# Performance work log

Measured on AMD Instinct MI355X. Metric: run time of the kernel, lower is better.

## Reference

```python
import jax, jax.numpy as jnp
import numpy as np

NUM_NODES = 200000
NUM_EDGES = 200000
NUM_GRAPHS = 2048
F_IN = 128
H = 64


def setup_inputs() -> dict:
    key = jax.random.key(0)
    ks = jax.random.split(key, 16)
    x = jax.random.normal(ks[0], (NUM_NODES, F_IN), dtype=jnp.float32)
    edge_index = jax.random.randint(ks[1], (2, NUM_EDGES), 0, NUM_NODES, dtype=jnp.int64)
    batch = jnp.sort(jax.random.randint(ks[2], (NUM_NODES,), 0, NUM_GRAPHS, dtype=jnp.int64))
    s_in = 1.0 / np.sqrt(F_IN)
    s_h = 1.0 / np.sqrt(H)
    W1a = jax.random.uniform(ks[3], (F_IN, H), jnp.float32, -s_in, s_in)
    b1a = jax.random.uniform(ks[4], (H,), jnp.float32, -s_in, s_in)
    W1b = jax.random.uniform(ks[5], (H, H), jnp.float32, -s_h, s_h)
    b1b = jax.random.uniform(ks[6], (H,), jnp.float32, -s_h, s_h)
    W2a = jax.random.uniform(ks[7], (H, H), jnp.float32, -s_h, s_h)
    b2a = jax.random.uniform(ks[8], (H,), jnp.float32, -s_h, s_h)
    W2b = jax.random.uniform(ks[9], (H, H), jnp.float32, -s_h, s_h)
    b2b = jax.random.uniform(ks[10], (H,), jnp.float32, -s_h, s_h)
    fcW = jax.random.uniform(ks[11], (H, 1), jnp.float32, -s_h, s_h)
    fcb = jax.random.uniform(ks[12], (1,), jnp.float32, -s_h, s_h)
    return {"x": x, "edge_index": edge_index, "batch": batch,
            "W1a": W1a, "b1a": b1a, "W1b": W1b, "b1b": b1b,
            "W2a": W2a, "b2a": b2a, "W2b": W2b, "b2b": b2b,
            "fcW": fcW, "fcb": fcb}


def gin_conv(h, edge_index, Wa, ba, Wb, bb):
    # sum aggregation: messages from source (row 0) scattered to target (row 1)
    msgs = h[edge_index[0]]  # [E, D]
    agg = jax.ops.segment_sum(msgs, edge_index[1], num_segments=NUM_NODES)
    z = h + agg  # eps = 0 default: (1+eps)*x + sum_j x_j
    z = jnp.maximum(z @ Wa + ba, 0.0)
    return z @ Wb + bb


def reference(x, edge_index, batch, W1a, b1a, W1b, b1b, W2a, b2a, W2b, b2b, fcW, fcb):
    h = jnp.maximum(gin_conv(x, edge_index, W1a, b1a, W1b, b1b), 0.0)
    h = jnp.maximum(gin_conv(h, edge_index, W2a, b2a, W2b, b2b), 0.0)
    # global mean pool per graph
    sums = jax.ops.segment_sum(h, batch, num_segments=NUM_GRAPHS)  # [G, H]
    counts = jax.ops.segment_sum(jnp.ones((h.shape[0],), h.dtype), batch, num_segments=NUM_GRAPHS)
    pooled = sums / jnp.maximum(counts, 1.0)[:, None]
    out = pooled @ fcW + fcb  # [G, 1]
    return out.squeeze(-1)
```

## Files before the change

### kernel.cpp

```cpp
#include <hip/hip_runtime.h>
#include <hip/hip_bf16.h>


#define NODES 200000
#define NPAD  200064
#define EDGES 200000
#define GRAPHS 2048
#define NB_SCAN 782

typedef __attribute__((ext_vector_type(8))) short short8;
typedef __attribute__((ext_vector_type(4))) float f32x4;

__device__ __forceinline__ unsigned short f2bf(float f) {
    unsigned u = __builtin_bit_cast(unsigned, f);
    u = (u + 0x7fffu + ((u >> 16) & 1u)) >> 16;
    return (unsigned short)u;
}
__device__ __forceinline__ float bf2f(unsigned short h) {
    unsigned u = ((unsigned)h) << 16;
    return __builtin_bit_cast(float, u);
}

__global__ __launch_bounds__(256) void count_k(
    const int* __restrict__ ei, int* __restrict__ cnt, int E)
{
    int e = blockIdx.x * 256 + threadIdx.x;
    if (e < E) atomicAdd(&cnt[ei[E + e]], 1);
}

__global__ __launch_bounds__(256) void scan1_k(
    const int* __restrict__ cnt, int* __restrict__ excl,
    int* __restrict__ bsum, int N)
{
    __shared__ int sh[256];
    int tid = threadIdx.x;
    int i = blockIdx.x * 256 + tid;
    int v = (i < N) ? cnt[i] : 0;
    sh[tid] = v;
    __syncthreads();
    for (int off = 1; off < 256; off <<= 1) {
        int t = (tid >= off) ? sh[tid - off] : 0;
        __syncthreads();
        sh[tid] += t;
        __syncthreads();
    }
    if (i < N) excl[i] = sh[tid] - v;
    if (tid == 255) bsum[blockIdx.x] = sh[255];
}

__global__ __launch_bounds__(1024) void scan2_k(int* __restrict__ bsum, int NB)
{
    __shared__ int sh[1024];
    int tid = threadIdx.x;
    int v = (tid < NB) ? bsum[tid] : 0;
    sh[tid] = v;
    __syncthreads();
    for (int off = 1; off < 1024; off <<= 1) {
        int t = (tid >= off) ? sh[tid - off] : 0;
        __syncthreads();
        sh[tid] += t;
        __syncthreads();
    }
    if (tid < NB) bsum[tid] = sh[tid] - v;
}

__global__ __launch_bounds__(256) void scan3_k(
    int* __restrict__ rowptr, const int* __restrict__ bsum,
    int* __restrict__ cursor, int N, int E)
{
    int i = blockIdx.x * 256 + threadIdx.x;
    if (i < N) {
        int v = rowptr[i] + bsum[blockIdx.x];
        rowptr[i] = v;
        cursor[i] = v;
    }
    if (i == 0) rowptr[N] = E;
}

__global__ __launch_bounds__(256) void fill_k(
    const int* __restrict__ ei, int* __restrict__ cursor,
    int* __restrict__ srcs, int E)
{
    int e = blockIdx.x * 256 + threadIdx.x;
    if (e < E) {
        int d = ei[E + e];
        int p = atomicAdd(&cursor[d], 1);
        srcs[p] = ei[e];
    }
}

__device__ __forceinline__ void wconv(const float* __restrict__ W,
                                      short* __restrict__ F, int e, int NE)
{
    int lane = e & 63, nb = (e >> 6) & 3, kc = e >> 8;
    int col = nb * 16 + (lane & 15);
    int kb = kc * 32 + ((lane >> 4) * 8);
    short8 hi, lo;
    #pragma unroll
    for (int j = 0; j < 8; ++j) {
        float w = W[(size_t)(kb + j) * 64 + col];
        unsigned short h = f2bf(w);
        float r = w - bf2f(h);
        hi[j] = (short)h;
        lo[j] = (short)f2bf(r);
    }
    *reinterpret_cast<short8*>(F + (size_t)e * 8) = hi;
    *reinterpret_cast<short8*>(F + (size_t)NE * 8 + (size_t)e * 8) = lo;
}

__global__ __launch_bounds__(256) void wsplit_k(
    const float* __restrict__ W1a, const float* __restrict__ W1b,
    const float* __restrict__ W2a, const float* __restrict__ W2b,
    short* __restrict__ F1a, short* __restrict__ F1b,
    short* __restrict__ F2a, short* __restrict__ F2b)
{
    int t = blockIdx.x * 256 + threadIdx.x;
    if (t < 1024)      wconv(W1a, F1a, t, 1024);
    else if (t < 1536) wconv(W1b, F1b, t - 1024, 512);
    else if (t < 2048) wconv(W2a, F2a, t - 1536, 512);
    else if (t < 2560) wconv(W2b, F2b, t - 2048, 512);
}

__device__ __forceinline__ void cvt_a8(const float4& a, const float4& b,
                                       short8& hi, short8& lo)
{
    float av[8] = {a.x, a.y, a.z, a.w, b.x, b.y, b.z, b.w};
    #pragma unroll
    for (int j = 0; j < 8; ++j) {
        unsigned short h = f2bf(av[j]);
        float r = av[j] - bf2f(h);
        hi[j] = (short)h;
        lo[j] = (short)f2bf(r);
    }
}

__global__ __launch_bounds__(256) void mm1_k(
    const float* __restrict__ A, const short* __restrict__ Wf,
    float* __restrict__ out, int N)
{
    const int tid = threadIdx.x;
    const int lane = tid & 63;
    const int wv = tid >> 6;
    const int row0w = blockIdx.x * 128 + wv * 32;
    const int grp = lane >> 4, c = lane & 15;
    const int koff = grp * 8;

    const float* Ar0 = A + (size_t)min(row0w + c, N - 1) * 128;
    const float* Ar1 = A + (size_t)min(row0w + 16 + c, N - 1) * 128;

    f32x4 acc[2][4];
    #pragma unroll
    for (int rg = 0; rg < 2; ++rg)
        #pragma unroll
        for (int nb = 0; nb < 4; ++nb)
            acc[rg][nb] = (f32x4){0.f, 0.f, 0.f, 0.f};

    #pragma unroll
    for (int kc = 0; kc < 4; ++kc) {
        const int kb = kc * 32 + koff;
        float4 a00 = *reinterpret_cast<const float4*>(Ar0 + kb);
        float4 a01 = *reinterpret_cast<const float4*>(Ar0 + kb + 4);
        float4 a10 = *reinterpret_cast<const float4*>(Ar1 + kb);
        float4 a11 = *reinterpret_cast<const float4*>(Ar1 + kb + 4);
        short8 h0, l0, h1, l1;
        cvt_a8(a00, a01, h0, l0);
        cvt_a8(a10, a11, h1, l1);
        #pragma unroll
        for (int nb = 0; nb < 4; ++nb) {
            short8 whi = *reinterpret_cast<const short8*>(Wf + ((size_t)((kc * 4 + nb) * 64) + lane) * 8);
            short8 wlo = *reinterpret_cast<const short8*>(Wf + ((size_t)(1024 + (kc * 4 + nb) * 64) + lane) * 8);
            acc[0][nb] = __builtin_amdgcn_mfma_f32_16x16x32_bf16(h0, whi, acc[0][nb], 0, 0, 0);
            acc[0][nb] = __builtin_amdgcn_mfma_f32_16x16x32_bf16(l0, whi, acc[0][nb], 0, 0, 0);
            acc[0][nb] = __builtin_amdgcn_mfma_f32_16x16x32_bf16(h0, wlo, acc[0][nb], 0, 0, 0);
            acc[1][nb] = __builtin_amdgcn_mfma_f32_16x16x32_bf16(h1, whi, acc[1][nb], 0, 0, 0);
            acc[1][nb] = __builtin_amdgcn_mfma_f32_16x16x32_bf16(l1, whi, acc[1][nb], 0, 0, 0);
            acc[1][nb] = __builtin_amdgcn_mfma_f32_16x16x32_bf16(h1, wlo, acc[1][nb], 0, 0, 0);
        }
    }

    #pragma unroll
    for (int rg = 0; rg < 2; ++rg)
        #pragma unroll
        for (int nb = 0; nb < 4; ++nb)
            #pragma unroll
            for (int reg = 0; reg < 4; ++reg)
                out[(size_t)(row0w + rg * 16 + grp * 4 + reg) * 64 + nb * 16 + c] = acc[rg][nb][reg];
}

__device__ __forceinline__ void agg_frag16(
    const float* __restrict__ y, const int* __restrict__ rowptr,
    const int* __restrict__ srcs, const float* __restrict__ bias,
    int n, int koff, bool valid, short8 fh[2], short8 fl[2])
{
    if (!valid) {
        #pragma unroll
        for (int i = 0; i < 8; ++i) {
            fh[0][i] = 0; fl[0][i] = 0; fh[1][i] = 0; fl[1][i] = 0;
        }
        return;
    }
    float a[16];
    {
        const float* yr = y + (size_t)n * 64;
        float4 a0 = *reinterpret_cast<const float4*>(yr + koff);
        float4 a1 = *reinterpret_cast<const float4*>(yr + koff + 4);
        float4 a2 = *reinterpret_cast<const float4*>(yr + 32 + koff);
        float4 a3 = *reinterpret_cast<const float4*>(yr + 32 + koff + 4);
        float4 b0 = *reinterpret_cast<const float4*>(bias + koff);
        float4 b1 = *reinterpret_cast<const float4*>(bias + koff + 4);
        float4 b2 = *reinterpret_cast<const float4*>(bias + 32 + koff);
        float4 b3 = *reinterpret_cast<const float4*>(bias + 32 + koff + 4);
        a[0] = a0.x + b0.x;  a[1] = a0.y + b0.y;  a[2] = a0.z + b0.z;  a[3] = a0.w + b0.w;
        a[4] = a1.x + b1.x;  a[5] = a1.y + b1.y;  a[6] = a1.z + b1.z;  a[7] = a1.w + b1.w;
        a[8] = a2.x + b2.x;  a[9] = a2.y + b2.y;  a[10] = a2.z + b2.z; a[11] = a2.w + b2.w;
        a[12] = a3.x + b3.x; a[13] = a3.y + b3.y; a[14] = a3.z + b3.z; a[15] = a3.w + b3.w;
    }
    int s0 = rowptr[n], s1 = rowptr[n + 1];
    for (int j = s0; j < s1; ++j) {
        const float* ys = y + (size_t)srcs[j] * 64;
        float4 v0 = *reinterpret_cast<const float4*>(ys + koff);
        float4 v1 = *reinterpret_cast<const float4*>(ys + koff + 4);
        float4 v2 = *reinterpret_cast<const float4*>(ys + 32 + koff);
        float4 v3 = *reinterpret_cast<const float4*>(ys + 32 + koff + 4);
        a[0] += v0.x;  a[1] += v0.y;  a[2] += v0.z;  a[3] += v0.w;
        a[4] += v1.x;  a[5] += v1.y;  a[6] += v1.z;  a[7] += v1.w;
        a[8] += v2.x;  a[9] += v2.y;  a[10] += v2.z; a[11] += v2.w;
        a[12] += v3.x; a[13] += v3.y; a[14] += v3.z; a[15] += v3.w;
    }
    #pragma unroll
    for (int i = 0; i < 16; ++i) {
        float v = fmaxf(a[i], 0.f);
        unsigned short h = f2bf(v);
        float r = v - bf2f(h);
        fh[i >> 3][i & 7] = (short)h;
        fl[i >> 3][i & 7] = (short)f2bf(r);
    }
}

__global__ __launch_bounds__(256) void mmaggmm_k(
    const float* __restrict__ y, const int* __restrict__ rowptr,
    const int* __restrict__ srcs, const float* __restrict__ bagg,
    const short* __restrict__ Wf1, const float* __restrict__ b1,
    const short* __restrict__ Wf2, float* __restrict__ out, int N)
{
    __shared__ short hT[4][32 * 72];
    __shared__ short lT[4][32 * 72];
    const int tid = threadIdx.x;
    const int lane = tid & 63;
    const int wv = tid >> 6;
    const int row0w = blockIdx.x * 128 + wv * 32;
    const int grp = lane >> 4, c = lane & 15;
    const int koff = grp * 8;

    short8 fh0[2], fl0[2], fh1[2], fl1[2];
    {
        int n0 = row0w + c;
        int n1 = row0w + 16 + c;
        agg_frag16(y, rowptr, srcs, bagg, n0, koff, n0 < N, fh0, fl0);
        agg_frag16(y, rowptr, srcs, bagg, n1, koff, n1 < N, fh1, fl1);
    }

    f32x4 acc[2][4];
    #pragma unroll
    for (int rg = 0; rg < 2; ++rg)
        #pragma unroll
        for (int nb = 0; nb < 4; ++nb)
            acc[rg][nb] = (f32x4){0.f, 0.f, 0.f, 0.f};

    #pragma unroll
    for (int kc = 0; kc < 2; ++kc) {
        #pragma unroll
        for (int nb = 0; nb < 4; ++nb) {
            short8 whi = *reinterpret_cast<const short8*>(Wf1 + ((size_t)((kc * 4 + nb) * 64) + lane) * 8);
            short8 wlo = *reinterpret_cast<const short8*>(Wf1 + ((size_t)(512 + (kc * 4 + nb) * 64) + lane) * 8);
            acc[0][nb] = __builtin_amdgcn_mfma_f32_16x16x32_bf16(fh0[kc], whi, acc[0][nb], 0, 0, 0);
            acc[0][nb] = __builtin_amdgcn_mfma_f32_16x16x32_bf16(fl0[kc], whi, acc[0][nb], 0, 0, 0);
            acc[0][nb] = __builtin_amdgcn_mfma_f32_16x16x32_bf16(fh0[kc], wlo, acc[0][nb], 0, 0, 0);
            acc[1][nb] = __builtin_amdgcn_mfma_f32_16x16x32_bf16(fh1[kc], whi, acc[1][nb], 0, 0, 0);
            acc[1][nb] = __builtin_amdgcn_mfma_f32_16x16x32_bf16(fl1[kc], whi, acc[1][nb], 0, 0, 0);
            acc[1][nb] = __builtin_amdgcn_mfma_f32_16x16x32_bf16(fh1[kc], wlo, acc[1][nb], 0, 0, 0);
        }
    }

    #pragma unroll
    for (int rg = 0; rg < 2; ++rg)
        #pragma unroll
        for (int nb = 0; nb < 4; ++nb) {
            const int col = nb * 16 + c;
            const float bv = b1[col];
            #pragma unroll
            for (int reg = 0; reg < 4; ++reg) {
                const int lr = rg * 16 + grp * 4 + reg;
                float v = fmaxf(acc[rg][nb][reg] + bv, 0.f);
                unsigned short h = f2bf(v);
                float r = v - bf2f(h);
                hT[wv][lr * 72 + col] = (short)h;
                lT[wv][lr * 72 + col] = (short)f2bf(r);
            }
        }
    __syncthreads();

    f32x4 acc2[2][4];
    #pragma unroll
    for (int rg = 0; rg < 2; ++rg)
        #pragma unroll
        for (int nb = 0; nb < 4; ++nb)
            acc2[rg][nb] = (f32x4){0.f, 0.f, 0.f, 0.f};

    #pragma unroll
    for (int kc = 0; kc < 2; ++kc) {
        const int kb = kc * 32 + koff;
        short8 h0 = *reinterpret_cast<const short8*>(&hT[wv][(0 + c) * 72 + kb]);
        short8 l0 = *reinterpret_cast<const short8*>(&lT[wv][(0 + c) * 72 + kb]);
        short8 h1 = *reinterpret_cast<const short8*>(&hT[wv][(16 + c) * 72 + kb]);
        short8 l1 = *reinterpret_cast<const short8*>(&lT[wv][(16 + c) * 72 + kb]);
        #pragma unroll
        for (int nb = 0; nb < 4; ++nb) {
            short8 whi = *reinterpret_cast<const short8*>(Wf2 + ((size_t)((kc * 4 + nb) * 64) + lane) * 8);
            short8 wlo = *reinterpret_cast<const short8*>(Wf2 + ((size_t)(512 + (kc * 4 + nb) * 64) + lane) * 8);
            acc2[0][nb] = __builtin_amdgcn_mfma_f32_16x16x32_bf16(h0, whi, acc2[0][nb], 0, 0, 0);
            acc2[0][nb] = __builtin_amdgcn_mfma_f32_16x16x32_bf16(l0, whi, acc2[0][nb], 0, 0, 0);
            acc2[0][nb] = __builtin_amdgcn_mfma_f32_16x16x32_bf16(h0, wlo, acc2[0][nb], 0, 0, 0);
            acc2[1][nb] = __builtin_amdgcn_mfma_f32_16x16x32_bf16(h1, whi, acc2[1][nb], 0, 0, 0);
            acc2[1][nb] = __builtin_amdgcn_mfma_f32_16x16x32_bf16(l1, whi, acc2[1][nb], 0, 0, 0);
            acc2[1][nb] = __builtin_amdgcn_mfma_f32_16x16x32_bf16(h1, wlo, acc2[1][nb], 0, 0, 0);
        }
    }

    #pragma unroll
    for (int rg = 0; rg < 2; ++rg)
        #pragma unroll
        for (int nb = 0; nb < 4; ++nb)
            #pragma unroll
            for (int reg = 0; reg < 4; ++reg)
                out[(size_t)(row0w + rg * 16 + grp * 4 + reg) * 64 + nb * 16 + c] = acc2[rg][nb][reg];
}

__global__ __launch_bounds__(256) void mmaggpool_k(
    const float* __restrict__ y, const int* __restrict__ rowptr,
    const int* __restrict__ srcs, const float* __restrict__ bagg,
    const short* __restrict__ Wf, const float* __restrict__ bias,
    const float* __restrict__ fcW, const int* __restrict__ batch,
    float* __restrict__ gacc, int N)
{
    __shared__ float rd[4][32];
    __shared__ int bls[4][32];
    const int tid = threadIdx.x;
    const int lane = tid & 63;
    const int wv = tid >> 6;
    const int row0w = blockIdx.x * 128 + wv * 32;
    const int grp = lane >> 4, c = lane & 15;
    const int koff = grp * 8;

    short8 fh0[2], fl0[2], fh1[2], fl1[2];
    {
        int n0 = row0w + c;
        int n1 = row0w + 16 + c;
        agg_frag16(y, rowptr, srcs, bagg, n0, koff, n0 < N, fh0, fl0);
        agg_frag16(y, rowptr, srcs, bagg, n1, koff, n1 < N, fh1, fl1);
    }

    f32x4 acc[2][4];
    #pragma unroll
    for (int rg = 0; rg < 2; ++rg)
        #pragma unroll
        for (int nb = 0; nb < 4; ++nb)
            acc[rg][nb] = (f32x4){0.f, 0.f, 0.f, 0.f};

    #pragma unroll
    for (int kc = 0; kc < 2; ++kc) {
        #pragma unroll
        for (int nb = 0; nb < 4; ++nb) {
            short8 whi = *reinterpret_cast<const short8*>(Wf + ((size_t)((kc * 4 + nb) * 64) + lane) * 8);
            short8 wlo = *reinterpret_cast<const short8*>(Wf + ((size_t)(512 + (kc * 4 + nb) * 64) + lane) * 8);
            acc[0][nb] = __builtin_amdgcn_mfma_f32_16x16x32_bf16(fh0[kc], whi, acc[0][nb], 0, 0, 0);
            acc[0][nb] = __builtin_amdgcn_mfma_f32_16x16x32_bf16(fl0[kc], whi, acc[0][nb], 0, 0, 0);
            acc[0][nb] = __builtin_amdgcn_mfma_f32_16x16x32_bf16(fh0[kc], wlo, acc[0][nb], 0, 0, 0);
            acc[1][nb] = __builtin_amdgcn_mfma_f32_16x16x32_bf16(fh1[kc], whi, acc[1][nb], 0, 0, 0);
            acc[1][nb] = __builtin_amdgcn_mfma_f32_16x16x32_bf16(fl1[kc], whi, acc[1][nb], 0, 0, 0);
            acc[1][nb] = __builtin_amdgcn_mfma_f32_16x16x32_bf16(fh1[kc], wlo, acc[1][nb], 0, 0, 0);
        }
    }

    float bv[4], fw[4];
    #pragma unroll
    for (int nb = 0; nb < 4; ++nb) {
        bv[nb] = bias[nb * 16 + c];
        fw[nb] = fcW[nb * 16 + c];
    }
    if (lane < 32) bls[wv][lane] = batch[min(row0w + lane, N - 1)];

    #pragma unroll
    for (int rg = 0; rg < 2; ++rg)
        #pragma unroll
        for (int reg = 0; reg < 4; ++reg) {
            float t = 0.f;
            #pragma unroll
            for (int nb = 0; nb < 4; ++nb)
                t += fmaxf(acc[rg][nb][reg] + bv[nb], 0.f) * fw[nb];
            t += __shfl_xor(t, 1, 16);
            t += __shfl_xor(t, 2, 16);
            t += __shfl_xor(t, 4, 16);
            t += __shfl_xor(t, 8, 16);
            if (c == 0) rd[wv][rg * 16 + grp * 4 + reg] = t;
        }

    if (lane == 0) {
        int cnt = min(32, N - row0w);
        if (cnt > 0) {
            int curg = bls[wv][0];
            float s = rd[wv][0];
            for (int i = 1; i < cnt; ++i) {
                int g = bls[wv][i];
                float v = rd[wv][i];
                if (g == curg) s += v;
                else { atomicAdd(&gacc[curg], s); curg = g; s = v; }
            }
            atomicAdd(&gacc[curg], s);
        }
    }
}

__global__ __launch_bounds__(256) void finalize_k(
    const float* __restrict__ gacc, const int* __restrict__ batch,
    const float* __restrict__ fcb, float* __restrict__ out, int N, int G)
{
    int g = blockIdx.x * 256 + threadIdx.x;
    if (g >= G) return;
    int lo = 0, hi = N;
    while (lo < hi) { int m = (lo + hi) >> 1; if (batch[m] < g) lo = m + 1; else hi = m; }
    int start = lo;
    hi = N;
    while (lo < hi) { int m = (lo + hi) >> 1; if (batch[m] < g + 1) lo = m + 1; else hi = m; }
    float cnt = fmaxf((float)(lo - start), 1.f);
    out[g] = gacc[g] / cnt + fcb[0];
}

extern "C" void kernel_launch(void* const* d_in, const int* in_sizes, int n_in,
                              void* d_out, int out_size, void* d_ws, size_t ws_size,
                              hipStream_t stream)
{
    const float* x     = (const float*)d_in[0];
    const int*   ei    = (const int*)d_in[1];
    const int*   batch = (const int*)d_in[2];
    const float* W1a   = (const float*)d_in[3];
    const float* b1a   = (const float*)d_in[4];
    const float* W1b   = (const float*)d_in[5];
    const float* b1b   = (const float*)d_in[6];
    const float* W2a   = (const float*)d_in[7];
    const float* b2a   = (const float*)d_in[8];
    const float* W2b   = (const float*)d_in[9];
    const float* b2b   = (const float*)d_in[10];
    const float* fcW   = (const float*)d_in[11];
    const float* fcb   = (const float*)d_in[12];
    float* out = (float*)d_out;

    const int N = NODES, E = EDGES, G = GRAPHS;
    char* ws = (char*)d_ws;

    float* y1 = (float*)ws;
    float* y2 = (float*)(ws + (size_t)NPAD * 64 * 4);
    char*  rest = ws + 2 * (size_t)NPAD * 64 * 4;
    int* cnt    = (int*)rest;
    int* rowptr = cnt + NODES;
    int* cursor = rowptr + NODES + 1;
    int* srcs   = cursor + NODES;
    int* bsum   = srcs + EDGES;
    float* gacc = (float*)(bsum + NB_SCAN + 2);
    short* F1a  = (short*)(((size_t)(gacc + GRAPHS) + 63) & ~(size_t)63);
    short* F1b  = F1a + 2 * 1024 * 8;
    short* F2a  = F1b + 2 * 512 * 8;
    short* F2b  = F2a + 2 * 512 * 8;

    const int NBLK = NPAD / 128;

    hipMemsetAsync(cnt, 0, (size_t)N * sizeof(int), stream);
    hipMemsetAsync(gacc, 0, (size_t)G * sizeof(float), stream);
    count_k<<<NB_SCAN, 256, 0, stream>>>(ei, cnt, E);
    scan1_k<<<NB_SCAN, 256, 0, stream>>>(cnt, rowptr, bsum, N);
    scan2_k<<<1, 1024, 0, stream>>>(bsum, NB_SCAN);
    scan3_k<<<NB_SCAN, 256, 0, stream>>>(rowptr, bsum, cursor, N, E);
    fill_k<<<NB_SCAN, 256, 0, stream>>>(ei, cursor, srcs, E);
    wsplit_k<<<10, 256, 0, stream>>>(W1a, W1b, W2a, W2b, F1a, F1b, F2a, F2b);

    mm1_k<<<NBLK, 256, 0, stream>>>(x, F1a, y1, N);

    mmaggmm_k<<<NBLK, 256, 0, stream>>>(y1, rowptr, srcs, b1a, F1b, b1b, F2a, y2, N);

    mmaggpool_k<<<NBLK, 256, 0, stream>>>(y2, rowptr, srcs, b2a, F2b, b2b, fcW, batch, gacc, N);
    finalize_k<<<(G + 255) / 256, 256, 0, stream>>>(gacc, batch, fcb, out, N, G);
}
```

Before: 306.4 us.

## Fuse setup memsets and weight split, merge scan stages, unroll gather loop

Replaces two memsets and the weight-split kernel with one setup kernel, and merges the single-block second scan into the third scan so each block sums the preceding block totals itself. The neighbor-gather loop now handles two edges per iteration to put more loads in flight, and the batch-id load in the pool kernel moves earlier. Together these cut the launch count by three, at the cost of every scan block redundantly reading up to 782 partial sums.

Measured after the change: 290.7 us. -5.1%, faster.

```diff
diff --git a/kernel.cpp b/kernel.cpp
--- a/kernel.cpp
+++ b/kernel.cpp
@@ -19,6 +19,41 @@
 __device__ __forceinline__ float bf2f(unsigned short h) {
     unsigned u = ((unsigned)h) << 16;
     return __builtin_bit_cast(float, u);
+}
+
+__device__ __forceinline__ void wconv(const float* __restrict__ W,
+                                      short* __restrict__ F, int e, int NE)
+{
+    int lane = e & 63, nb = (e >> 6) & 3, kc = e >> 8;
+    int col = nb * 16 + (lane & 15);
+    int kb = kc * 32 + ((lane >> 4) * 8);
+    short8 hi, lo;
+    #pragma unroll
+    for (int j = 0; j < 8; ++j) {
+        float w = W[(size_t)(kb + j) * 64 + col];
+        unsigned short h = f2bf(w);
+        float r = w - bf2f(h);
+        hi[j] = (short)h;
+        lo[j] = (short)f2bf(r);
+    }
+    *reinterpret_cast<short8*>(F + (size_t)e * 8) = hi;
+    *reinterpret_cast<short8*>(F + (size_t)NE * 8 + (size_t)e * 8) = lo;
+}
+
+__global__ __launch_bounds__(256) void setup_k(
+    const float* __restrict__ W1a, const float* __restrict__ W1b,
+    const float* __restrict__ W2a, const float* __restrict__ W2b,
+    short* __restrict__ F1a, short* __restrict__ F1b,
+    short* __restrict__ F2a, short* __restrict__ F2b,
+    int* __restrict__ cnt, float* __restrict__ gacc)
+{
+    int t = blockIdx.x * 256 + threadIdx.x;
+    if (t < NODES) cnt[t] = 0;
+    if (t < GRAPHS) gacc[t] = 0.f;
+    if (t < 1024)      wconv(W1a, F1a, t, 1024);
+    else if (t < 1536) wconv(W1b, F1b, t - 1024, 512);
+    else if (t < 2048) wconv(W2a, F2a, t - 1536, 512);
+    else if (t < 2560) wconv(W2b, F2b, t - 2048, 512);
 }
 
 __global__ __launch_bounds__(256) void count_k(
@@ -48,29 +83,24 @@
     if (tid == 255) bsum[blockIdx.x] = sh[255];
 }
 
-__global__ __launch_bounds__(1024) void scan2_k(int* __restrict__ bsum, int NB)
-{
-    __shared__ int sh[1024];
-    int tid = threadIdx.x;
-    int v = (tid < NB) ? bsum[tid] : 0;
-    sh[tid] = v;
-    __syncthreads();
-    for (int off = 1; off < 1024; off <<= 1) {
-        int t = (tid >= off) ? sh[tid - off] : 0;
-        __syncthreads();
-        sh[tid] += t;
-        __syncthreads();
-    }
-    if (tid < NB) bsum[tid] = sh[tid] - v;
-}
-
-__global__ __launch_bounds__(256) void scan3_k(
+__global__ __launch_bounds__(256) void scan23_k(
     int* __restrict__ rowptr, const int* __restrict__ bsum,
     int* __restrict__ cursor, int N, int E)
 {
-    int i = blockIdx.x * 256 + threadIdx.x;
+    __shared__ int wsum[4];
+    __shared__ int soff;
+    int tid = threadIdx.x;
+    int partial = 0;
+    for (int b = tid; b < blockIdx.x; b += 256) partial += bsum[b];
+    #pragma unroll
+    for (int off = 32; off >= 1; off >>= 1) partial += __shfl_down(partial, off);
+    if ((tid & 63) == 0) wsum[tid >> 6] = partial;
+    __syncthreads();
+    if (tid == 0) soff = wsum[0] + wsum[1] + wsum[2] + wsum[3];
+    __syncthreads();
+    int i = blockIdx.x * 256 + tid;
     if (i < N) {
-        int v = rowptr[i] + bsum[blockIdx.x];
+        int v = rowptr[i] + soff;
         rowptr[i] = v;
         cursor[i] = v;
     }
@@ -87,38 +117,6 @@
         int p = atomicAdd(&cursor[d], 1);
         srcs[p] = ei[e];
     }
-}
-
-__device__ __forceinline__ void wconv(const float* __restrict__ W,
-                                      short* __restrict__ F, int e, int NE)
-{
-    int lane = e & 63, nb = (e >> 6) & 3, kc = e >> 8;
-    int col = nb * 16 + (lane & 15);
-    int kb = kc * 32 + ((lane >> 4) * 8);
-    short8 hi, lo;
-    #pragma unroll
-    for (int j = 0; j < 8; ++j) {
-        float w = W[(size_t)(kb + j) * 64 + col];
-        unsigned short h = f2bf(w);
-        float r = w - bf2f(h);
-        hi[j] = (short)h;
-        lo[j] = (short)f2bf(r);
-    }
-    *reinterpret_cast<short8*>(F + (size_t)e * 8) = hi;
-    *reinterpret_cast<short8*>(F + (size_t)NE * 8 + (size_t)e * 8) = lo;
-}
-
-__global__ __launch_bounds__(256) void wsplit_k(
-    const float* __restrict__ W1a, const float* __restrict__ W1b,
-    const float* __restrict__ W2a, const float* __restrict__ W2b,
-    short* __restrict__ F1a, short* __restrict__ F1b,
-    short* __restrict__ F2a, short* __restrict__ F2b)
-{
-    int t = blockIdx.x * 256 + threadIdx.x;
-    if (t < 1024)      wconv(W1a, F1a, t, 1024);
-    else if (t < 1536) wconv(W1b, F1b, t - 1024, 512);
-    else if (t < 2048) wconv(W2a, F2a, t - 1536, 512);
-    else if (t < 2560) wconv(W2b, F2b, t - 2048, 512);
 }
 
 __device__ __forceinline__ void cvt_a8(const float4& a, const float4& b,
@@ -216,7 +214,28 @@
         a[12] = a3.x + b3.x; a[13] = a3.y + b3.y; a[14] = a3.z + b3.z; a[15] = a3.w + b3.w;
     }
     int s0 = rowptr[n], s1 = rowptr[n + 1];
-    for (int j = s0; j < s1; ++j) {
+    int j = s0;
+    for (; j + 2 <= s1; j += 2) {
+        const float* ysA = y + (size_t)srcs[j] * 64;
+        const float* ysB = y + (size_t)srcs[j + 1] * 64;
+        float4 A0 = *reinterpret_cast<const float4*>(ysA + koff);
+        float4 A1 = *reinterpret_cast<const float4*>(ysA + koff + 4);
+        float4 A2 = *reinterpret_cast<const float4*>(ysA + 32 + koff);
+        float4 A3 = *reinterpret_cast<const float4*>(ysA + 32 + koff + 4);
+        float4 B0 = *reinterpret_cast<const float4*>(ysB + koff);
+        float4 B1 = *reinterpret_cast<const float4*>(ysB + koff + 4);
+        float4 B2 = *reinterpret_cast<const float4*>(ysB + 32 + koff);
+        float4 B3 = *reinterpret_cast<const float4*>(ysB + 32 + koff + 4);
+        a[0] += A0.x;  a[1] += A0.y;  a[2] += A0.z;  a[3] += A0.w;
+        a[4] += A1.x;  a[5] += A1.y;  a[6] += A1.z;  a[7] += A1.w;
+        a[8] += A2.x;  a[9] += A2.y;  a[10] += A2.z; a[11] += A2.w;
+        a[12] += A3.x; a[13] += A3.y; a[14] += A3.z; a[15] += A3.w;
+        a[0] += B0.x;  a[1] += B0.y;  a[2] += B0.z;  a[3] += B0.w;
+        a[4] += B1.x;  a[5] += B1.y;  a[6] += B1.z;  a[7] += B1.w;
+        a[8] += B2.x;  a[9] += B2.y;  a[10] += B2.z; a[11] += B2.w;
+        a[12] += B3.x; a[13] += B3.y; a[14] += B3.z; a[15] += B3.w;
+    }
+    if (j < s1) {
         const float* ys = y + (size_t)srcs[j] * 64;
         float4 v0 = *reinterpret_cast<const float4*>(ys + koff);
         float4 v1 = *reinterpret_cast<const float4*>(ys + koff + 4);
@@ -352,6 +371,8 @@
     const int grp = lane >> 4, c = lane & 15;
     const int koff = grp * 8;
 
+    if (lane < 32) bls[wv][lane] = batch[min(row0w + lane, N - 1)];
+
     short8 fh0[2], fl0[2], fh1[2], fl1[2];
     {
         int n0 = row0w + c;
@@ -388,7 +409,6 @@
         bv[nb] = bias[nb * 16 + c];
         fw[nb] = fcW[nb * 16 + c];
     }
-    if (lane < 32) bls[wv][lane] = batch[min(row0w + lane, N - 1)];
 
     #pragma unroll
     for (int rg = 0; rg < 2; ++rg)
@@ -474,14 +494,11 @@
 
     const int NBLK = NPAD / 128;
 
-    hipMemsetAsync(cnt, 0, (size_t)N * sizeof(int), stream);
-    hipMemsetAsync(gacc, 0, (size_t)G * sizeof(float), stream);
+    setup_k<<<NB_SCAN, 256, 0, stream>>>(W1a, W1b, W2a, W2b, F1a, F1b, F2a, F2b, cnt, gacc);
     count_k<<<NB_SCAN, 256, 0, stream>>>(ei, cnt, E);
     scan1_k<<<NB_SCAN, 256, 0, stream>>>(cnt, rowptr, bsum, N);
-    scan2_k<<<1, 1024, 0, stream>>>(bsum, NB_SCAN);
-    scan3_k<<<NB_SCAN, 256, 0, stream>>>(rowptr, bsum, cursor, N, E);
+    scan23_k<<<NB_SCAN, 256, 0, stream>>>(rowptr, bsum, cursor, N, E);
     fill_k<<<NB_SCAN, 256, 0, stream>>>(ei, cursor, srcs, E);
-    wsplit_k<<<10, 256, 0, stream>>>(W1a, W1b, W2a, W2b, F1a, F1b, F2a, F2b);
 
     mm1_k<<<NBLK, 256, 0, stream>>>(x, F1a, y1, N);
 
```
